# Performance work log

Hardware: AMD Instinct MI355X
Metric: run time of the kernel (lower is better)

The kernel has to match this reference:

```python
import jax, jax.numpy as jnp
import numpy as np

B, T, E = 2, 1024, 1024
H, HD = 8, 128            # n_heads, head_dim
WS = 64                   # window_size (< T -> sliding-window branch)
TAU = 10.0
SCALE = 1.0 / np.sqrt(HD)


def setup_inputs() -> dict:
    key = jax.random.key(0)
    ks = jax.random.split(key, 8)
    s = 0.02
    return {
        "h": jax.random.normal(ks[0], (B, T, E), jnp.float32),
        "coord_1d": jax.random.uniform(ks[1], (B, T), jnp.float32),
        "Wq_w": jax.random.normal(ks[2], (E, E), jnp.float32) * s,
        "Wq_b": jnp.zeros((E,), jnp.float32),
        "Wk_w": jax.random.normal(ks[3], (E, E), jnp.float32) * s,
        "Wk_b": jnp.zeros((E,), jnp.float32),
        "Wv_w": jax.random.normal(ks[4], (E, E), jnp.float32) * s,
        "Wv_b": jnp.zeros((E,), jnp.float32),
        "Wo_w": jax.random.normal(ks[5], (E, E), jnp.float32) * s,
        "Wo_b": jnp.zeros((E,), jnp.float32),
    }


def reference(h, coord_1d, Wq_w, Wq_b, Wk_w, Wk_b, Wv_w, Wv_b, Wo_w, Wo_b):
    # sort positions by 1-D coordinate
    sort_idx = jnp.argsort(coord_1d, axis=1)          # (B,T)
    inv_idx = jnp.argsort(sort_idx, axis=1)
    h_s = jnp.take_along_axis(h, sort_idx[:, :, None], axis=1)  # (B,T,E)
    c_s = jnp.take_along_axis(coord_1d, sort_idx, axis=1)       # (B,T)

    def proj(w, b):
        return (h_s @ w.T + b).reshape(B, T, H, HD).transpose(0, 2, 1, 3)  # (B,H,T,HD)

    Q, K, V = proj(Wq_w, Wq_b), proj(Wk_w, Wk_b), proj(Wv_w, Wv_b)

    # centered sliding-window indices, clamped at sequence edges: (T, WS)
    pos = jnp.arange(T)
    start = jnp.clip(pos - WS // 2, 0, None)
    overflow = jnp.clip(start + WS - T, 0, None)
    start = jnp.clip(start - overflow, 0, None)
    base_idx = start[:, None] + jnp.arange(WS)

    # sorted-sequence position of depot (original index 0)
    depot = jnp.argmax(sort_idx == 0, axis=1)         # (B,)

    # append forced depot column -> (B,T,WS+1)
    idx_ext = jnp.concatenate(
        [jnp.broadcast_to(base_idx[None], (B, T, WS)),
         jnp.broadcast_to(depot[:, None, None], (B, T, 1))], axis=2)
    has_depot = jnp.any(base_idx[None] == depot[:, None, None], axis=2)  # (B,T)
    keep = jnp.concatenate(
        [jnp.ones((B, T, WS), bool), (~has_depot)[:, :, None]], axis=2)  # (B,T,WS+1)

    # gather windowed K/V: (B,H,T,WS+1,HD)
    gather_kv = jax.vmap(lambda x, idx: x[:, idx, :])
    K_w = gather_kv(K, idx_ext)
    V_w = gather_kv(V, idx_ext)

    scores = jnp.einsum('bhtd,bhtwd->bhtw', Q, K_w) * SCALE
    c_w = jax.vmap(lambda c, idx: c[idx])(c_s, idx_ext)          # (B,T,WS+1)
    dist2 = (c_w - c_s[:, :, None]) ** 2
    scores = scores - dist2[:, None] / TAU
    neg = jnp.finfo(scores.dtype).min
    scores = jnp.where(keep[:, None], scores, neg)
    attn = jax.nn.softmax(scores, axis=-1)
    ctx = jnp.einsum('bhtw,bhtwd->bhtd', attn, V_w)
    local_out = ctx.transpose(0, 2, 1, 3).reshape(B, T, E) @ Wo_w.T + Wo_b

    # depot attends to the full sequence
    Qd = jax.vmap(lambda q, d: q[:, d, :])(Q, depot)             # (B,H,HD)
    sd = jnp.einsum('bhd,bhtd->bht', Qd, K) * SCALE
    cd = jnp.take_along_axis(c_s, depot[:, None], axis=1)        # (B,1)
    sd = sd - ((c_s - cd) ** 2)[:, None] / TAU
    ad = jax.nn.softmax(sd, axis=-1)
    ctxd = jnp.einsum('bht,bhtd->bhd', ad, V).reshape(B, E) @ Wo_w.T + Wo_b

    out_sorted = local_out.at[jnp.arange(B), depot].set(ctxd)
    return jnp.take_along_axis(out_sorted, inv_idx[:, :, None], axis=1)
```

## Files before the change

kernel.cpp:

```cpp
#include <hip/hip_runtime.h>
#include <hip/hip_bf16.h>
#include <cmath>

constexpr int BB_ = 2;
constexpr int T_  = 1024;
constexpr int E_  = 1024;
constexpr int H_  = 8;
constexpr int HD_ = 128;
constexpr int WS_ = 64;
constexpr float TAU_   = 10.0f;
constexpr float SCALE_ = 0.08838834764831843f;

typedef __attribute__((ext_vector_type(8))) _Float16 half8;
typedef __attribute__((ext_vector_type(4))) _Float16 half4;
typedef __attribute__((ext_vector_type(2))) _Float16 half2v;
typedef __attribute__((ext_vector_type(4))) float floatx4;

constexpr int STB_ = 16;

__global__ __launch_bounds__(256) void sort_rank_kernel(
    const float* __restrict__ coord, int* __restrict__ sidx,
    float* __restrict__ c_s, int* __restrict__ depot) {
  __shared__ float c[T_];
  const int nb = T_ / STB_;
  const int b = blockIdx.x / nb;
  const int t0 = (blockIdx.x % nb) * STB_;
  const float* cb = coord + (size_t)b * T_;
  for (int i = threadIdx.x; i < T_; i += 256) c[i] = cb[i];
  __syncthreads();
  const int tl = threadIdx.x >> 4;
  const int ch = threadIdx.x & 15;
  const int t = t0 + tl;
  const float ct = c[t];
  int rank = 0;
  const int u0 = ch * (T_ / 16);
  #pragma unroll 8
  for (int i = 0; i < T_ / 16; ++i) {
    const int u = u0 + i;
    const float cu = c[u];
    rank += (cu < ct) || (cu == ct && u < t);
  }
  #pragma unroll
  for (int o = 8; o > 0; o >>= 1) rank += __shfl_xor(rank, o);
  if (ch == 0) {
    sidx[b * T_ + rank] = t;
    c_s[b * T_ + rank] = ct;
    if (t == 0) depot[b] = rank;
  }
}

struct WConv {
  const float* src[4];
  _Float16* dst[4];
};

__global__ __launch_bounds__(256) void convert_w_kernel(WConv a) {
  const int z = blockIdx.z;
  const size_t idx = ((size_t)blockIdx.x * 256 + threadIdx.x) * 4;
  const float4 v = *(const float4*)(a.src[z] + idx);
  half4 hv;
  hv.x = (_Float16)v.x; hv.y = (_Float16)v.y;
  hv.z = (_Float16)v.z; hv.w = (_Float16)v.w;
  *(half4*)(a.dst[z] + idx) = hv;
}

struct GemmArgs {
  const _Float16* W[3];
  const float* bias[3];
  float* Cf[3];
  _Float16* Ch[3];
};

constexpr int LP_ = 56;

template <int BM, int BN, int GATHER, int SCATTER, int FP16OUT>
__global__ __launch_bounds__(256, 2) void gemm_f16(
    GemmArgs args, const void* __restrict__ Av, const int* __restrict__ sidx) {
  constexpr int TMI = BM / 32;
  constexpr int TNI = BN / 32;
  const _Float16* __restrict__ W = args.W[blockIdx.z];
  const float* __restrict__ bias = args.bias[blockIdx.z];

  __shared__ _Float16 As[BM][LP_], Bs[BN][LP_];
  __shared__ int srow[BM];

  const int tid = threadIdx.x;
  const int wv = tid >> 6, lane = tid & 63;
  const int kq = lane >> 4, ln15 = lane & 15;
  const int wm0 = (wv >> 1) * (BM / 2), wn0 = (wv & 1) * (BN / 2);
  const int m0 = blockIdx.y * BM, n0 = blockIdx.x * BN;

  if (GATHER) {
    if (tid < BM) {
      const int gr = m0 + tid;
      srow[tid] = (gr & ~(T_ - 1)) + sidx[gr];
    }
    __syncthreads();
  }

  floatx4 acc[TMI][TNI];
  #pragma unroll
  for (int i = 0; i < TMI; ++i)
    #pragma unroll
    for (int j = 0; j < TNI; ++j) acc[i][j] = (floatx4){0.f, 0.f, 0.f, 0.f};

  for (int k0 = 0; k0 < E_; k0 += 32) {
    if (GATHER) {
      const float* A = (const float*)Av;
      #pragma unroll
      for (int i = 0; i < BM * 8 / 256; ++i) {
        const int idx = tid + 256 * i;
        const int r = idx >> 3, c4 = idx & 7;
        const float4 v =
            *(const float4*)(A + (size_t)srow[r] * E_ + k0 + c4 * 4);
        half4 hv;
        hv.x = (_Float16)v.x; hv.y = (_Float16)v.y;
        hv.z = (_Float16)v.z; hv.w = (_Float16)v.w;
        *(half4*)&As[r][c4 * 4] = hv;
      }
    } else {
      const _Float16* A = (const _Float16*)Av;
      #pragma unroll
      for (int i = 0; i < BM * 4 / 256; ++i) {
        const int idx = tid + 256 * i;
        const int r = idx >> 2, c = idx & 3;
        *(half8*)&As[r][c * 8] =
            *(const half8*)(A + (size_t)(m0 + r) * E_ + k0 + c * 8);
      }
    }
    #pragma unroll
    for (int i = 0; i < BN * 4 / 256; ++i) {
      const int idx = tid + 256 * i;
      const int r = idx >> 2, c = idx & 3;
      *(half8*)&Bs[r][c * 8] =
          *(const half8*)(W + (size_t)(n0 + r) * E_ + k0 + c * 8);
    }
    __syncthreads();

    half8 ah[TMI], bf[TNI];
    #pragma unroll
    for (int mi = 0; mi < TMI; ++mi)
      ah[mi] = *(const half8*)&As[wm0 + mi * 16 + ln15][kq * 8];
    #pragma unroll
    for (int ni = 0; ni < TNI; ++ni)
      bf[ni] = *(const half8*)&Bs[wn0 + ni * 16 + ln15][kq * 8];
    #pragma unroll
    for (int mi = 0; mi < TMI; ++mi)
      #pragma unroll
      for (int ni = 0; ni < TNI; ++ni)
        acc[mi][ni] = __builtin_amdgcn_mfma_f32_16x16x32_f16(
            ah[mi], bf[ni], acc[mi][ni], 0, 0, 0);
    __syncthreads();
  }

  float* __restrict__ Cf = args.Cf[blockIdx.z];
  _Float16* __restrict__ Ch = args.Ch[blockIdx.z];
  #pragma unroll
  for (int ni = 0; ni < TNI; ++ni) {
    const int col = n0 + wn0 + ni * 16 + ln15;
    const float bv = bias[col];
    #pragma unroll
    for (int mi = 0; mi < TMI; ++mi) {
      #pragma unroll
      for (int r = 0; r < 4; ++r) {
        const int m = m0 + wm0 + mi * 16 + kq * 4 + r;
        const int orow = SCATTER ? ((m & ~(T_ - 1)) + sidx[m]) : m;
        const float val = acc[mi][ni][r] + bv;
        if (FP16OUT) {
          Ch[(size_t)orow * E_ + col] = (_Float16)val;
        } else {
          Cf[(size_t)orow * E_ + col] = val;
        }
      }
    }
  }
}

constexpr int QTm_ = 16;
constexpr int NSL_ = 80;
constexpr int VSP_ = 8;

__global__ __launch_bounds__(256) void attn_local_kernel(
    const _Float16* __restrict__ Qh, const _Float16* __restrict__ Kh,
    const _Float16* __restrict__ Vh, const float* __restrict__ c_s,
    const int* __restrict__ depot, _Float16* __restrict__ CTh,
    float* __restrict__ scg) {
  __shared__ float sc[QTm_][88];
  __shared__ float cw[NSL_];
  __shared__ float cq[QTm_];
  __shared__ float kdep[HD_];
  __shared__ float qdep[HD_];

  const int tid = threadIdx.x;
  const int ntq = T_ / QTm_;
  const int tq = blockIdx.x % ntq;
  const int bh = blockIdx.x / ntq;
  const int h = bh % H_, b = bh / H_;
  const int t0 = tq * QTm_;
  const int dep = depot[b];
  const int smin = min(max(t0 - 32, 0), T_ - WS_);
  const size_t baseBH = ((size_t)b * T_) * E_ + (size_t)h * HD_;

  if (tid < NSL_) {
    cw[tid] = c_s[b * T_ + min(smin + tid, T_ - 1)];
  } else if (tid < NSL_ + QTm_) {
    cq[tid - NSL_] = c_s[b * T_ + t0 + tid - NSL_];
  } else if (tid >= 128) {
    const int d = tid - 128;
    kdep[d] = (float)Kh[baseBH + (size_t)dep * E_ + d];
  }
  if (tid < HD_) qdep[tid] = (float)Qh[baseBH + (size_t)dep * E_ + tid];
  __syncthreads();

  const int wv = tid >> 6, lane = tid & 63;
  const int ln15 = lane & 15, kq = lane >> 4;

  {
    const size_t qoff = baseBH + (size_t)(t0 + ln15) * E_ + kq * 8;
    half8 aH[4];
    #pragma unroll
    for (int ks = 0; ks < 4; ++ks)
      aH[ks] = *(const half8*)(Qh + qoff + ks * 32);
    for (int kt = wv; kt < 5; kt += 4) {
      const int key = min(smin + kt * 16 + ln15, T_ - 1);
      const size_t koff = baseBH + (size_t)key * E_ + kq * 8;
      floatx4 acc = (floatx4){0.f, 0.f, 0.f, 0.f};
      #pragma unroll
      for (int ks = 0; ks < 4; ++ks) {
        const half8 b8 = *(const half8*)(Kh + koff + ks * 32);
        acc = __builtin_amdgcn_mfma_f32_16x16x32_f16(aH[ks], b8, acc, 0, 0, 0);
      }
      #pragma unroll
      for (int r = 0; r < 4; ++r)
        sc[kq * 4 + r][kt * 16 + ln15] = acc[r];
    }
  }

  const float cdep = c_s[b * T_ + dep];

  #pragma unroll
  for (int qi = 0; qi < 4; ++qi) {
    const int q = wv * 4 + qi;
    const int t = t0 + q;
    const size_t qo2 = baseBH + (size_t)t * E_;
    const float q1 = (float)Qh[qo2 + lane];
    const float q2 = (float)Qh[qo2 + 64 + lane];
    float part = fmaf(q1, kdep[lane], q2 * kdep[lane + 64]);
    #pragma unroll
    for (int o = 32; o > 0; o >>= 1) part += __shfl_xor(part, o);
    if (lane == 0) {
      const int st = min(max(t - 32, 0), T_ - WS_);
      const bool masked = (unsigned)(dep - st) < (unsigned)WS_;
      const float dd = cdep - cq[q];
      sc[q][80] = masked ? -3.0e38f
                         : part * SCALE_ - dd * dd * (1.0f / TAU_);
    }
  }

  #pragma unroll
  for (int qi = 0; qi < 4; ++qi) {
    const int k = t0 + wv * 4 + qi;
    const size_t ko = baseBH + (size_t)k * E_;
    const float k1 = (float)Kh[ko + lane];
    const float k2 = (float)Kh[ko + 64 + lane];
    float part = fmaf(qdep[lane], k1, qdep[lane + 64] * k2);
    #pragma unroll
    for (int o = 32; o > 0; o >>= 1) part += __shfl_xor(part, o);
    if (lane == 0) {
      const float dd = cw[k - smin] - cdep;
      scg[bh * T_ + k] = part * SCALE_ - dd * dd * (1.0f / TAU_);
    }
  }
  __syncthreads();

  #pragma unroll
  for (int qi = 0; qi < 4; ++qi) {
    const int q = wv * 4 + qi;
    const int t = t0 + q;
    const int st = min(max(t - 32, 0), T_ - WS_);
    const int base = st - smin;
    const float cqv = cq[q];
    const int j1 = lane;
    float s1 = -3.0e38f;
    if (j1 >= base && j1 < base + WS_) {
      const float dd = cw[j1] - cqv;
      s1 = sc[q][j1] * SCALE_ - dd * dd * (1.0f / TAU_);
    }
    const int j2 = 64 + lane;
    float s2 = -3.0e38f;
    if (lane < 16 && j2 >= base && j2 < base + WS_) {
      const float dd = cw[j2] - cqv;
      s2 = sc[q][j2] * SCALE_ - dd * dd * (1.0f / TAU_);
    }
    const float sdep = sc[q][80];
    float m = fmaxf(s1, s2);
    #pragma unroll
    for (int o = 32; o > 0; o >>= 1) m = fmaxf(m, __shfl_xor(m, o));
    m = fmaxf(m, sdep);
    const float e1 = expf(s1 - m);
    const float e2 = (lane < 16) ? expf(s2 - m) : 0.f;
    float sum = e1 + e2;
    #pragma unroll
    for (int o = 32; o > 0; o >>= 1) sum += __shfl_xor(sum, o);
    const float edep = expf(sdep - m);
    sum += edep;
    const float inv = 1.0f / sum;
    sc[q][j1] = e1 * inv;
    if (lane < 16) sc[q][j2] = e2 * inv;
    if (lane == 0) sc[q][80] = edep * inv;
  }
  __syncthreads();

  {
    const int dp = lane * 2;
    float acc0[4], acc1[4];
    #pragma unroll
    for (int qi = 0; qi < 4; ++qi) { acc0[qi] = 0.f; acc1[qi] = 0.f; }
    for (int j = 0; j <= NSL_; ++j) {
      const int row = (j < NSL_) ? min(smin + j, T_ - 1) : dep;
      const half2v v = *(const half2v*)(Vh + baseBH + (size_t)row * E_ + dp);
      const float v1 = (float)v.x;
      const float v2 = (float)v.y;
      #pragma unroll
      for (int qi = 0; qi < 4; ++qi) {
        const float w = sc[wv * 4 + qi][j];
        acc0[qi] = fmaf(w, v1, acc0[qi]);
        acc1[qi] = fmaf(w, v2, acc1[qi]);
      }
    }
    #pragma unroll
    for (int qi = 0; qi < 4; ++qi) {
      const int t = t0 + wv * 4 + qi;
      half2v o;
      o.x = (_Float16)acc0[qi];
      o.y = (_Float16)acc1[qi];
      *(half2v*)(CTh + baseBH + (size_t)t * E_ + dp) = o;
    }
  }
}

__global__ __launch_bounds__(256) void depot_ctx_kernel(
    const _Float16* __restrict__ Vh, const float* __restrict__ scg,
    float* __restrict__ part) {
  __shared__ float sc[T_];
  __shared__ float red[4];
  __shared__ float par[2][HD_];
  const int sp = blockIdx.x % VSP_;
  const int bh = blockIdx.x / VSP_;
  const int h = bh % H_, b = bh / H_;
  const int tid = threadIdx.x, wv = tid >> 6, lane = tid & 63;
  const float* s = scg + bh * T_;

  float lm = -3.0e38f;
  for (int k = tid; k < T_; k += 256) { sc[k] = s[k]; lm = fmaxf(lm, sc[k]); }
  #pragma unroll
  for (int o = 32; o > 0; o >>= 1) lm = fmaxf(lm, __shfl_xor(lm, o));
  if (lane == 0) red[wv] = lm;
  __syncthreads();
  const float M = fmaxf(fmaxf(red[0], red[1]), fmaxf(red[2], red[3]));
  __syncthreads();
  float ls = 0.f;
  float ev[T_ / 256];
  #pragma unroll
  for (int i = 0; i < T_ / 256; ++i) {
    ev[i] = expf(sc[tid + 256 * i] - M);
    ls += ev[i];
  }
  #pragma unroll
  for (int o = 32; o > 0; o >>= 1) ls += __shfl_xor(ls, o);
  if (lane == 0) red[wv] = ls;
  __syncthreads();
  const float inv = 1.0f / (red[0] + red[1] + red[2] + red[3]);
  #pragma unroll
  for (int i = 0; i < T_ / 256; ++i) sc[tid + 256 * i] = ev[i] * inv;
  __syncthreads();

  const int d = tid & 127, kg = tid >> 7;
  const size_t baseBH = ((size_t)b * T_) * E_ + (size_t)h * HD_;
  constexpr int KPB = T_ / VSP_;
  const int k0 = sp * KPB + kg * (KPB / 2);
  const _Float16* vbase = Vh + baseBH + d;
  float acc = 0.f;
  #pragma unroll 8
  for (int k = k0; k < k0 + KPB / 2; ++k) {
    acc = fmaf(sc[k], (float)vbase[(size_t)k * E_], acc);
  }
  par[kg][d] = acc;
  __syncthreads();
  if (tid < HD_) part[((size_t)sp * BB_ * H_ + bh) * HD_ + tid] =
      par[0][tid] + par[1][tid];
}

__global__ __launch_bounds__(256) void depot_write_kernel(
    const float* __restrict__ part, const int* __restrict__ depot,
    _Float16* __restrict__ CTh) {
  for (int o = threadIdx.x; o < BB_ * H_ * HD_; o += 256) {
    const int bh = o >> 7, d = o & 127;
    float s = 0.f;
    #pragma unroll
    for (int sp = 0; sp < VSP_; ++sp)
      s += part[((size_t)sp * BB_ * H_ + bh) * HD_ + d];
    const int h = bh % H_, b = bh / H_;
    const int dep = depot[b];
    CTh[((size_t)b * T_ + dep) * E_ + (size_t)h * HD_ + d] = (_Float16)s;
  }
}

extern "C" void kernel_launch(void* const* d_in, const int* in_sizes, int n_in,
                              void* d_out, int out_size, void* d_ws, size_t ws_size,
                              hipStream_t stream) {
  const float* h     = (const float*)d_in[0];
  const float* coord = (const float*)d_in[1];
  const float* Wq    = (const float*)d_in[2];
  const float* Wqb   = (const float*)d_in[3];
  const float* Wk    = (const float*)d_in[4];
  const float* Wkb   = (const float*)d_in[5];
  const float* Wv    = (const float*)d_in[6];
  const float* Wvb   = (const float*)d_in[7];
  const float* Wo    = (const float*)d_in[8];
  const float* Wob   = (const float*)d_in[9];
  float* out = (float*)d_out;

  char* ws = (char*)d_ws;
  const size_t MATH_ = (size_t)BB_ * T_ * E_ * 2;
  const size_t WB   = (size_t)E_ * E_ * 2;
  size_t off = 0;
  _Float16* Qh  = (_Float16*)(ws + off); off += MATH_;
  _Float16* Kh  = (_Float16*)(ws + off); off += MATH_;
  _Float16* Vh  = (_Float16*)(ws + off); off += MATH_;
  _Float16* CTh = (_Float16*)(ws + off); off += MATH_;
  _Float16* Wh[4];
  for (int i = 0; i < 4; ++i) { Wh[i] = (_Float16*)(ws + off); off += WB; }
  float* c_s = (float*)(ws + off); off += (size_t)BB_ * T_ * 4;
  int* sidx  = (int*)(ws + off);   off += (size_t)BB_ * T_ * 4;
  int* depo  = (int*)(ws + off);   off += 256;
  float* scg  = (float*)(ws + off); off += (size_t)BB_ * H_ * T_ * 4;
  float* dpar = (float*)(ws + off); off += (size_t)VSP_ * BB_ * H_ * HD_ * 4;

  sort_rank_kernel<<<BB_ * (T_ / STB_), 256, 0, stream>>>(coord, sidx, c_s, depo);

  WConv wc;
  wc.src[0] = Wq; wc.src[1] = Wk; wc.src[2] = Wv; wc.src[3] = Wo;
  for (int i = 0; i < 4; ++i) wc.dst[i] = Wh[i];
  convert_w_kernel<<<dim3(E_ * E_ / 1024, 1, 4), 256, 0, stream>>>(wc);

  GemmArgs qa;
  qa.W[0] = Wh[0]; qa.W[1] = Wh[1]; qa.W[2] = Wh[2];
  qa.bias[0] = Wqb; qa.bias[1] = Wkb; qa.bias[2] = Wvb;
  qa.Cf[0] = qa.Cf[1] = qa.Cf[2] = nullptr;
  qa.Ch[0] = Qh; qa.Ch[1] = Kh; qa.Ch[2] = Vh;
  gemm_f16<128, 64, 1, 0, 1><<<dim3(E_ / 64, (BB_ * T_) / 128, 3), 256, 0, stream>>>(
      qa, h, sidx);

  attn_local_kernel<<<BB_ * H_ * (T_ / QTm_), 256, 0, stream>>>(
      Qh, Kh, Vh, c_s, depo, CTh, scg);

  depot_ctx_kernel<<<BB_ * H_ * VSP_, 256, 0, stream>>>(Vh, scg, dpar);
  depot_write_kernel<<<1, 256, 0, stream>>>(dpar, depo, CTh);

  GemmArgs oa;
  oa.W[0] = oa.W[1] = oa.W[2] = Wh[3];
  oa.bias[0] = oa.bias[1] = oa.bias[2] = Wob;
  oa.Cf[0] = oa.Cf[1] = oa.Cf[2] = out;
  oa.Ch[0] = oa.Ch[1] = oa.Ch[2] = nullptr;
  gemm_f16<64, 64, 0, 1, 0><<<dim3(E_ / 64, (BB_ * T_) / 64, 1), 256, 0, stream>>>(
      oa, CTh, sidx);
}
```

Measured before the change: 169.4 us.

## Merge sort and weight conversion into one prep kernel, pre-scatter h to fp16

Sorting, fp32-to-fp16 weight conversion, and a new scatter of h into sorted fp16 rows are merged into one combined prep kernel launch. The QKV GEMM now reads a contiguous fp16 A matrix instead of gathering fp32 rows through sidx and converting them inside its K loop. This removes one launch and shrinks the GEMM's A-side traffic and conversion work. The cost is an extra 4 MB fp16 buffer plus an extra write and read pass over h.

```diff
diff --git a/kernel.cpp b/kernel.cpp
--- a/kernel.cpp
+++ b/kernel.cpp
@@ -17,51 +17,76 @@
 typedef __attribute__((ext_vector_type(4))) float floatx4;
 
 constexpr int STB_ = 16;
-
-__global__ __launch_bounds__(256) void sort_rank_kernel(
-    const float* __restrict__ coord, int* __restrict__ sidx,
-    float* __restrict__ c_s, int* __restrict__ depot) {
+constexpr int SORTB_ = BB_ * (T_ / STB_);
+constexpr int WCONVB_ = (E_ * E_) / (256 * 8);
+
+struct ComboArgs {
+  const float* coord;
+  const float* h;
+  int* sidx;
+  float* c_s;
+  int* depot;
+  _Float16* Ah;
+  const float* wsrc[4];
+  _Float16* wdst[4];
+};
+
+__global__ __launch_bounds__(256) void combo_prep_kernel(ComboArgs a) {
   __shared__ float c[T_];
-  const int nb = T_ / STB_;
-  const int b = blockIdx.x / nb;
-  const int t0 = (blockIdx.x % nb) * STB_;
-  const float* cb = coord + (size_t)b * T_;
-  for (int i = threadIdx.x; i < T_; i += 256) c[i] = cb[i];
-  __syncthreads();
-  const int tl = threadIdx.x >> 4;
-  const int ch = threadIdx.x & 15;
-  const int t = t0 + tl;
-  const float ct = c[t];
-  int rank = 0;
-  const int u0 = ch * (T_ / 16);
-  #pragma unroll 8
-  for (int i = 0; i < T_ / 16; ++i) {
-    const int u = u0 + i;
-    const float cu = c[u];
-    rank += (cu < ct) || (cu == ct && u < t);
-  }
-  #pragma unroll
-  for (int o = 8; o > 0; o >>= 1) rank += __shfl_xor(rank, o);
-  if (ch == 0) {
-    sidx[b * T_ + rank] = t;
-    c_s[b * T_ + rank] = ct;
-    if (t == 0) depot[b] = rank;
-  }
-}
-
-struct WConv {
-  const float* src[4];
-  _Float16* dst[4];
-};
-
-__global__ __launch_bounds__(256) void convert_w_kernel(WConv a) {
-  const int z = blockIdx.z;
-  const size_t idx = ((size_t)blockIdx.x * 256 + threadIdx.x) * 4;
-  const float4 v = *(const float4*)(a.src[z] + idx);
-  half4 hv;
-  hv.x = (_Float16)v.x; hv.y = (_Float16)v.y;
-  hv.z = (_Float16)v.z; hv.w = (_Float16)v.w;
-  *(half4*)(a.dst[z] + idx) = hv;
+  __shared__ int rnk[STB_];
+  const int tid = threadIdx.x;
+
+  if (blockIdx.x < SORTB_) {
+    const int nb = T_ / STB_;
+    const int b = blockIdx.x / nb;
+    const int t0 = (blockIdx.x % nb) * STB_;
+    const float* cb = a.coord + (size_t)b * T_;
+    for (int i = tid; i < T_; i += 256) c[i] = cb[i];
+    __syncthreads();
+    const int tl = tid >> 4;
+    const int ch = tid & 15;
+    const int t = t0 + tl;
+    const float ct = c[t];
+    int rank = 0;
+    const int u0 = ch * (T_ / 16);
+    #pragma unroll 8
+    for (int i = 0; i < T_ / 16; ++i) {
+      const int u = u0 + i;
+      const float cu = c[u];
+      rank += (cu < ct) || (cu == ct && u < t);
+    }
+    #pragma unroll
+    for (int o = 8; o > 0; o >>= 1) rank += __shfl_xor(rank, o);
+    if (ch == 0) {
+      a.sidx[b * T_ + rank] = t;
+      a.c_s[b * T_ + rank] = ct;
+      rnk[tl] = rank;
+      if (t == 0) a.depot[b] = rank;
+    }
+    __syncthreads();
+    #pragma unroll 4
+    for (int r = 0; r < STB_; ++r) {
+      const float4 v =
+          *(const float4*)(a.h + ((size_t)b * T_ + t0 + r) * E_ + tid * 4);
+      half4 hv;
+      hv.x = (_Float16)v.x; hv.y = (_Float16)v.y;
+      hv.z = (_Float16)v.z; hv.w = (_Float16)v.w;
+      *(half4*)(a.Ah + ((size_t)b * T_ + rnk[r]) * E_ + tid * 4) = hv;
+    }
+  } else {
+    const int wb = blockIdx.x - SORTB_;
+    const int z = wb / WCONVB_;
+    const int chunk = wb - z * WCONVB_;
+    const size_t idx = ((size_t)chunk * 256 + tid) * 8;
+    const float4 v0 = *(const float4*)(a.wsrc[z] + idx);
+    const float4 v1 = *(const float4*)(a.wsrc[z] + idx + 4);
+    half8 hv;
+    hv[0] = (_Float16)v0.x; hv[1] = (_Float16)v0.y;
+    hv[2] = (_Float16)v0.z; hv[3] = (_Float16)v0.w;
+    hv[4] = (_Float16)v1.x; hv[5] = (_Float16)v1.y;
+    hv[6] = (_Float16)v1.z; hv[7] = (_Float16)v1.w;
+    *(half8*)(a.wdst[z] + idx) = hv;
+  }
 }
 
 struct GemmArgs {
@@ -73,16 +98,16 @@
 
 constexpr int LP_ = 56;
 
-template <int BM, int BN, int GATHER, int SCATTER, int FP16OUT>
+template <int BM, int BN, int SCATTER, int FP16OUT>
 __global__ __launch_bounds__(256, 2) void gemm_f16(
-    GemmArgs args, const void* __restrict__ Av, const int* __restrict__ sidx) {
+    GemmArgs args, const _Float16* __restrict__ A,
+    const int* __restrict__ sidx) {
   constexpr int TMI = BM / 32;
   constexpr int TNI = BN / 32;
   const _Float16* __restrict__ W = args.W[blockIdx.z];
   const float* __restrict__ bias = args.bias[blockIdx.z];
 
   __shared__ _Float16 As[BM][LP_], Bs[BN][LP_];
-  __shared__ int srow[BM];
 
   const int tid = threadIdx.x;
   const int wv = tid >> 6, lane = tid & 63;
@@ -90,14 +115,6 @@
   const int wm0 = (wv >> 1) * (BM / 2), wn0 = (wv & 1) * (BN / 2);
   const int m0 = blockIdx.y * BM, n0 = blockIdx.x * BN;
 
-  if (GATHER) {
-    if (tid < BM) {
-      const int gr = m0 + tid;
-      srow[tid] = (gr & ~(T_ - 1)) + sidx[gr];
-    }
-    __syncthreads();
-  }
-
   floatx4 acc[TMI][TNI];
   #pragma unroll
   for (int i = 0; i < TMI; ++i)
@@ -105,28 +122,12 @@
     for (int j = 0; j < TNI; ++j) acc[i][j] = (floatx4){0.f, 0.f, 0.f, 0.f};
 
   for (int k0 = 0; k0 < E_; k0 += 32) {
-    if (GATHER) {
-      const float* A = (const float*)Av;
-      #pragma unroll
-      for (int i = 0; i < BM * 8 / 256; ++i) {
-        const int idx = tid + 256 * i;
-        const int r = idx >> 3, c4 = idx & 7;
-        const float4 v =
-            *(const float4*)(A + (size_t)srow[r] * E_ + k0 + c4 * 4);
-        half4 hv;
-        hv.x = (_Float16)v.x; hv.y = (_Float16)v.y;
-        hv.z = (_Float16)v.z; hv.w = (_Float16)v.w;
-        *(half4*)&As[r][c4 * 4] = hv;
-      }
-    } else {
-      const _Float16* A = (const _Float16*)Av;
-      #pragma unroll
-      for (int i = 0; i < BM * 4 / 256; ++i) {
-        const int idx = tid + 256 * i;
-        const int r = idx >> 2, c = idx & 3;
-        *(half8*)&As[r][c * 8] =
-            *(const half8*)(A + (size_t)(m0 + r) * E_ + k0 + c * 8);
-      }
+    #pragma unroll
+    for (int i = 0; i < BM * 4 / 256; ++i) {
+      const int idx = tid + 256 * i;
+      const int r = idx >> 2, c = idx & 3;
+      *(half8*)&As[r][c * 8] =
+          *(const half8*)(A + (size_t)(m0 + r) * E_ + k0 + c * 8);
     }
     #pragma unroll
     for (int i = 0; i < BN * 4 / 256; ++i) {
@@ -428,6 +429,7 @@
   _Float16* Qh  = (_Float16*)(ws + off); off += MATH_;
   _Float16* Kh  = (_Float16*)(ws + off); off += MATH_;
   _Float16* Vh  = (_Float16*)(ws + off); off += MATH_;
+  _Float16* Ah  = (_Float16*)(ws + off); off += MATH_;
   _Float16* CTh = (_Float16*)(ws + off); off += MATH_;
   _Float16* Wh[4];
   for (int i = 0; i < 4; ++i) { Wh[i] = (_Float16*)(ws + off); off += WB; }
@@ -437,20 +439,20 @@
   float* scg  = (float*)(ws + off); off += (size_t)BB_ * H_ * T_ * 4;
   float* dpar = (float*)(ws + off); off += (size_t)VSP_ * BB_ * H_ * HD_ * 4;
 
-  sort_rank_kernel<<<BB_ * (T_ / STB_), 256, 0, stream>>>(coord, sidx, c_s, depo);
-
-  WConv wc;
-  wc.src[0] = Wq; wc.src[1] = Wk; wc.src[2] = Wv; wc.src[3] = Wo;
-  for (int i = 0; i < 4; ++i) wc.dst[i] = Wh[i];
-  convert_w_kernel<<<dim3(E_ * E_ / 1024, 1, 4), 256, 0, stream>>>(wc);
+  ComboArgs ca;
+  ca.coord = coord; ca.h = h; ca.sidx = sidx; ca.c_s = c_s;
+  ca.depot = depo; ca.Ah = Ah;
+  ca.wsrc[0] = Wq; ca.wsrc[1] = Wk; ca.wsrc[2] = Wv; ca.wsrc[3] = Wo;
+  for (int i = 0; i < 4; ++i) ca.wdst[i] = Wh[i];
+  combo_prep_kernel<<<SORTB_ + 4 * WCONVB_, 256, 0, stream>>>(ca);
 
   GemmArgs qa;
   qa.W[0] = Wh[0]; qa.W[1] = Wh[1]; qa.W[2] = Wh[2];
   qa.bias[0] = Wqb; qa.bias[1] = Wkb; qa.bias[2] = Wvb;
   qa.Cf[0] = qa.Cf[1] = qa.Cf[2] = nullptr;
   qa.Ch[0] = Qh; qa.Ch[1] = Kh; qa.Ch[2] = Vh;
-  gemm_f16<128, 64, 1, 0, 1><<<dim3(E_ / 64, (BB_ * T_) / 128, 3), 256, 0, stream>>>(
-      qa, h, sidx);
+  gemm_f16<128, 64, 0, 1><<<dim3(E_ / 64, (BB_ * T_) / 128, 3), 256, 0, stream>>>(
+      qa, Ah, sidx);
 
   attn_local_kernel<<<BB_ * H_ * (T_ / QTm_), 256, 0, stream>>>(
       Qh, Kh, Vh, c_s, depo, CTh, scg);
@@ -463,6 +465,6 @@
   oa.bias[0] = oa.bias[1] = oa.bias[2] = Wob;
   oa.Cf[0] = oa.Cf[1] = oa.Cf[2] = out;
   oa.Ch[0] = oa.Ch[1] = oa.Ch[2] = nullptr;
-  gemm_f16<64, 64, 0, 1, 0><<<dim3(E_ / 64, (BB_ * T_) / 64, 1), 256, 0, stream>>>(
+  gemm_f16<64, 64, 1, 0><<<dim3(E_ / 64, (BB_ * T_) / 64, 1), 256, 0, stream>>>(
       oa, CTh, sidx);
 }
```

New measurement: 172.4 us. About the same (+1.7%).
